# Kernel tuning notes

Hardware: AMD Instinct MI355X
Metric: run time of the kernel (lower is better)

Reference implementation:

```python
import jax, jax.numpy as jnp
import numpy as np

B, CIN, COUT, H, W = 2, 128, 128, 128, 256
KH, KW = 3, 3
CMID = 32  # COUT // low_factor


def setup_inputs() -> dict:
    key = jax.random.key(0)
    ks = jax.random.split(key, 7)
    x = jax.random.normal(ks[0], (B, CIN, H, W), jnp.float32)
    # torchvision deform_conv2d offset layout: [2*KH*KW, Ho, Wo], (dy, dx) per tap
    offset = jax.random.normal(ks[1], (2 * KH * KW, H, W), jnp.float32)
    weight = jax.random.normal(ks[2], (COUT, CIN, KH, KW), jnp.float32) * 0.05
    bias = jax.random.normal(ks[3], (COUT,), jnp.float32) * 0.01
    down_w = jax.random.normal(ks[4], (CMID, 2 * COUT), jnp.float32) * 0.05
    up_w = jax.random.normal(ks[5], (COUT, CMID), jnp.float32) * 0.05
    scale = jnp.float32(1.0)
    return dict(x=x, offset=offset, weight=weight, bias=bias,
                down_w=down_w, up_w=up_w, scale=scale)


def _deform_conv2d(x, offset, weight, bias):
    # stride=1, padding=1, dilation=1, groups=1 (matches init_conv config)
    Bn, C, Hh, Ww = x.shape
    Co, _, kh, kw = weight.shape
    K = kh * kw
    Ho, Wo = offset.shape[-2:]
    off = offset.reshape(K, 2, Ho, Wo)
    dy, dx = off[:, 0], off[:, 1]                      # [K, Ho, Wo]
    ki, kj = jnp.meshgrid(jnp.arange(kh), jnp.arange(kw), indexing='ij')
    ki = ki.reshape(K).astype(jnp.float32)
    kj = kj.reshape(K).astype(jnp.float32)
    i = jnp.arange(Ho, dtype=jnp.float32)
    j = jnp.arange(Wo, dtype=jnp.float32)
    PAD = 1.0
    py = i[None, :, None] - PAD + ki[:, None, None] + dy   # [K, Ho, Wo]
    px = j[None, None, :] - PAD + kj[:, None, None] + dx
    y0 = jnp.floor(py).astype(jnp.int32)
    x0 = jnp.floor(px).astype(jnp.int32)
    fy = py - y0.astype(py.dtype)
    fx = px - x0.astype(px.dtype)
    xf = x.reshape(Bn, C, Hh * Ww)

    def gather(yi, xi, w):
        # zero padding outside the image (torchvision semantics)
        valid = (yi >= 0) & (yi < Hh) & (xi >= 0) & (xi < Ww)
        yc = jnp.clip(yi, 0, Hh - 1)
        xc = jnp.clip(xi, 0, Ww - 1)
        idx = (yc * Ww + xc).reshape(-1)                   # [K*Ho*Wo]
        g = xf[:, :, idx].reshape(Bn, C, K, Ho, Wo)
        return g * (w * valid.astype(w.dtype))[None, None]

    val = gather(y0, x0, (1.0 - fy) * (1.0 - fx))
    val = val + gather(y0, x0 + 1, (1.0 - fy) * fx)
    val = val + gather(y0 + 1, x0, fy * (1.0 - fx))
    val = val + gather(y0 + 1, x0 + 1, fy * fx)
    out = jnp.einsum('bcnij,ocn->boij', val, weight.reshape(Co, C, K))
    return out + bias[None, :, None, None]


def reference(x, offset, weight, bias, down_w, up_w, scale):
    # h = original frozen conv (weights shared with the deform branch, ablation != wo_copy)
    h = jax.lax.conv_general_dilated(
        x, weight, window_strides=(1, 1), padding=[(1, 1), (1, 1)],
        dimension_numbers=('NCHW', 'OIHW', 'NCHW'))
    h = h + bias[None, :, None, None]
    dx = _deform_conv2d(x, offset, weight, bias)
    dx = jnp.concatenate([dx, h], axis=1)                  # mix == 'cat'
    lo = jnp.einsum('bcij,dc->bdij', dx, down_w)           # 1x1 conv_down
    up = jnp.einsum('bcij,dc->bdij', lo, up_w)             # 1x1 conv_up
    return h + scale * up
```

## Files before the change

kernel.cpp:

```cpp
#include <hip/hip_runtime.h>
#include <hip/hip_bf16.h>

typedef __attribute__((ext_vector_type(8))) short short8;
typedef __attribute__((ext_vector_type(8))) unsigned short ushort8;
typedef __attribute__((ext_vector_type(4))) float f32x4;
typedef __attribute__((ext_vector_type(4))) int int4v;
typedef __attribute__((ext_vector_type(4))) float float4v;
typedef __attribute__((ext_vector_type(2))) float float2v;
typedef __attribute__((ext_vector_type(4))) unsigned int uint4v;

#define HH 128
#define WW 256
#define CIN_ 128
#define COUT_ 128

__device__ __forceinline__ unsigned short f2bf(float f) {
  union { __hip_bfloat16 h; unsigned short u; } v;
  v.h = __float2bfloat16(f);
  return v.u;
}

__global__ __launch_bounds__(256) void k_pre1(
    const float* __restrict__ down_w, const float* __restrict__ weight,
    float* __restrict__ T,
    const float* __restrict__ x, unsigned short* __restrict__ xh,
    const float* __restrict__ offset, int4v* __restrict__ mo,
    float4v* __restrict__ mw) {
  __shared__ float tile[32 * 129];
  int bid = blockIdx.x;
  int tid = threadIdx.x;

  if (bid < 288) {
    int e = bid * 256 + tid;
    if (e >= 2 * 32 * 1152) return;
    int s = e / 36864, r = e % 36864, d = r / 1152, ck = r % 1152;
    float a = 0.f;
    #pragma unroll 4
    for (int p = 0; p < 128; ++p)
      a += down_w[d * 256 + s * 128 + p] * weight[p * 1152 + ck];
    T[e] = a;
  } else if (bid < 2336) {
    int idx = bid - 288;
    int b = idx >> 10, rem = idx & 1023;
    int y = rem >> 3, xg = (rem & 7) << 5;
    for (int it = tid; it < 32 * 128; it += 256) {
      int c = it >> 5, xi = it & 31;
      tile[xi * 129 + c] = x[(((size_t)b * 128 + c) * 128 + y) * 256 + xg + xi];
    }
    __syncthreads();
    for (int it = tid; it < 32 * 16; it += 256) {
      int xi = it >> 4, cs = it & 15;
      ushort8 v;
      #pragma unroll
      for (int e = 0; e < 8; ++e) v[e] = f2bf(tile[xi * 129 + cs * 8 + e]);
      *(ushort8*)(xh + (((size_t)b * 128 + y) * 256 + xg + xi) * 128 + cs * 8) = v;
    }
  } else {
    int e = (bid - 2336) * 256 + tid;
    if (e >= 9 * 128 * 256) return;
    int k = e >> 15, rem = e & 32767;
    int ii = rem >> 8, jj = rem & 255;
    float dy = offset[(2 * k) * 32768 + rem];
    float dx = offset[(2 * k + 1) * 32768 + rem];
    int ki = k / 3, kj = k % 3;
    float py = (float)(ii - 1 + ki) + dy;
    float px = (float)(jj - 1 + kj) + dx;
    float fy0 = floorf(py), fx0 = floorf(px);
    int y0 = (int)fy0, x0 = (int)fx0;
    float fy = py - fy0, fx = px - fx0;
    int ys[2] = {y0, y0 + 1};
    int xs_[2] = {x0, x0 + 1};
    float wy[2] = {1.f - fy, fy}, wx[2] = {1.f - fx, fx};
    int4v o;
    float4v w;
    #pragma unroll
    for (int cy = 0; cy < 2; ++cy) {
      #pragma unroll
      for (int cx = 0; cx < 2; ++cx) {
        int yy = ys[cy], xx = xs_[cx];
        bool valid = (yy >= 0) && (yy < HH) && (xx < WW) && (xx >= 0);
        int yc = min(max(yy, 0), HH - 1), xc = min(max(xx, 0), WW - 1);
        int off = (yc * WW + xc) * CIN_;
        float wv = valid ? wy[cy] * wx[cx] : 0.f;
        int ci = cy * 2 + cx;
        if (ci == 0) { o.x = off; w.x = wv; }
        else if (ci == 1) { o.y = off; w.y = wv; }
        else if (ci == 2) { o.z = off; w.z = wv; }
        else { o.w = off; w.w = wv; }
      }
    }
    mo[e] = o;
    mw[e] = w;
  }
}

__global__ __launch_bounds__(256) void k_pre2(
    const float* __restrict__ up_w, const float* __restrict__ weight,
    const float* __restrict__ T, const float* __restrict__ scale,
    unsigned short* __restrict__ wdef, unsigned short* __restrict__ wstd,
    const float* __restrict__ down_w, const float* __restrict__ bias,
    float* __restrict__ beff) {
  __shared__ float sd[32];
  int bid = blockIdx.x;
  int t = threadIdx.x;
  if (bid < 1152) {
    int e = bid * 256 + t;
    if (e >= 2 * 9 * 128 * 128) return;
    int s = e / 147456, r = e % 147456;
    int tap = r / 16384, o = (r / 128) % 128, c = r % 128;
    int ck = c * 9 + tap;
    const float* Ts = T + s * 36864;
    float a = 0.f;
    #pragma unroll
    for (int d = 0; d < 32; ++d) a += up_w[o * 32 + d] * Ts[d * 1152 + ck];
    float scl = scale[0];
    int idx = ((tap * 4 + (c >> 5)) * 128 + o) * 32 + (c & 31);
    if (s == 1) {
      wstd[idx] = f2bf(weight[o * 1152 + ck] + scl * a);
    } else {
      wdef[idx] = f2bf(scl * a);
    }
  } else {
    if (t < 32) {
      float a = 0.f;
      for (int p = 0; p < 128; ++p)
        a += (down_w[t * 256 + p] + down_w[t * 256 + 128 + p]) * bias[p];
      sd[t] = a;
    }
    __syncthreads();
    if (t < 128) {
      float a = 0.f;
      #pragma unroll
      for (int d = 0; d < 32; ++d) a += up_w[t * 32 + d] * sd[d];
      beff[t] = bias[t] + scale[0] * a;
    }
  }
}

__global__ __launch_bounds__(512, 4) void k_main(
    const unsigned short* __restrict__ xh,
    const int4v* __restrict__ mo, const float4v* __restrict__ mw,
    const unsigned short* __restrict__ wstd, const unsigned short* __restrict__ wdef,
    const float* __restrict__ beff, float* __restrict__ out) {
  __shared__ __align__(16) unsigned short sbuf[2][64 * 128];

  int orig = blockIdx.x;
  int t = ((orig & 7) << 7) + (orig >> 3);
  int b = t >> 9, i = (t >> 2) & 127, j0 = (t & 3) << 6;
  int tid = threadIdx.x;
  const unsigned short* xb = xh + (size_t)b * (HH * WW * CIN_);

  int wid = tid >> 6;
  bool producer = wid < 4;

  if (producer) {
    int ptid = tid;
    int slot = ptid & 15, pg = ptid >> 4;
    int ce = slot * 8;

    auto COMB = [&](uint4v* g, float4v w, int q, unsigned short* buf) {
      int p = q * 16 + pg;
      uint4v r;
      #pragma unroll
      for (int wi = 0; wi < 4; ++wi) {
        unsigned u0 = g[0][wi], u1 = g[1][wi], u2 = g[2][wi], u3 = g[3][wi];
        float2v f0 = {__builtin_bit_cast(float, u0 << 16), __builtin_bit_cast(float, u0 & 0xffff0000u)};
        float2v f1 = {__builtin_bit_cast(float, u1 << 16), __builtin_bit_cast(float, u1 & 0xffff0000u)};
        float2v f2 = {__builtin_bit_cast(float, u2 << 16), __builtin_bit_cast(float, u2 & 0xffff0000u)};
        float2v f3 = {__builtin_bit_cast(float, u3 << 16), __builtin_bit_cast(float, u3 & 0xffff0000u)};
        float2v s = w.x * f0 + w.y * f1 + w.z * f2 + w.w * f3;
        unsigned rr;
        asm("v_cvt_pk_bf16_f32 %0, %1, %2" : "=v"(rr) : "v"(s.x), "v"(s.y));
        r[wi] = rr;
      }
      *(uint4v*)((char*)buf + (p << 8) + ((slot ^ (p & 15)) << 4)) = r;
    };

    auto STAGE_DEF = [&](int tap, unsigned short* buf) {
      int4v o;
      float4v wq0, wq1;
      uint4v g0[4], g1[4];
      int mbase = (tap * HH + i) * WW + j0 + pg;

      o = mo[mbase]; wq0 = mw[mbase];
      g0[0] = *(const uint4v*)(xb + o.x + ce);
      g0[1] = *(const uint4v*)(xb + o.y + ce);
      g0[2] = *(const uint4v*)(xb + o.z + ce);
      g0[3] = *(const uint4v*)(xb + o.w + ce);
      o = mo[mbase + 16]; wq1 = mw[mbase + 16];
      g1[0] = *(const uint4v*)(xb + o.x + ce);
      g1[1] = *(const uint4v*)(xb + o.y + ce);
      g1[2] = *(const uint4v*)(xb + o.z + ce);
      g1[3] = *(const uint4v*)(xb + o.w + ce);

      COMB(g0, wq0, 0, buf);
      o = mo[mbase + 32]; wq0 = mw[mbase + 32];
      g0[0] = *(const uint4v*)(xb + o.x + ce);
      g0[1] = *(const uint4v*)(xb + o.y + ce);
      g0[2] = *(const uint4v*)(xb + o.z + ce);
      g0[3] = *(const uint4v*)(xb + o.w + ce);
      COMB(g1, wq1, 1, buf);
      o = mo[mbase + 48]; wq1 = mw[mbase + 48];
      g1[0] = *(const uint4v*)(xb + o.x + ce);
      g1[1] = *(const uint4v*)(xb + o.y + ce);
      g1[2] = *(const uint4v*)(xb + o.z + ce);
      g1[3] = *(const uint4v*)(xb + o.w + ce);
      COMB(g0, wq0, 2, buf);
      COMB(g1, wq1, 3, buf);
    };

    auto STAGE_STD = [&](int tap, unsigned short* buf) {
      int ki = tap / 3, kj = tap % 3;
      int gy = i - 1 + ki;
      bool oky = (unsigned)gy < (unsigned)HH;
      uint4v s[4];
      #pragma unroll
      for (int q = 0; q < 4; ++q) {
        int p = q * 16 + pg;
        int gx = j0 + p - 1 + kj;
        uint4v vv = {};
        if (oky && (unsigned)gx < (unsigned)WW)
          vv = *(const uint4v*)(xb + (size_t)(gy * WW + gx) * CIN_ + ce);
        s[q] = vv;
      }
      #pragma unroll
      for (int q = 0; q < 4; ++q) {
        int p = q * 16 + pg;
        *(uint4v*)((char*)buf + (p << 8) + ((slot ^ (p & 15)) << 4)) = s[q];
      }
    };

    STAGE_STD(0, sbuf[0]);
    __syncthreads();
    for (int v = 0; v < 18; ++v) {
      if (v < 17) {
        int nv = v + 1;
        if (nv & 1) STAGE_DEF(nv >> 1, sbuf[nv & 1]);
        else        STAGE_STD(nv >> 1, sbuf[nv & 1]);
      }
      __syncthreads();
    }
  } else {
    int lane = tid & 63;
    int cw = wid - 4;
    int obase = cw << 5;
    int lrow = lane & 15, lhi = lane >> 4;

    f32x4 acc[2][4] = {};

    __syncthreads();
    for (int v = 0; v < 18; ++v) {
      const unsigned short* cur = sbuf[v & 1];
      const unsigned short* wt = ((v & 1) ? wdef : wstd) + (size_t)(v >> 1) * 16384;
      short8 af[4][2];
      #pragma unroll
      for (int cc = 0; cc < 4; ++cc)
        #pragma unroll
        for (int am = 0; am < 2; ++am)
          af[cc][am] = *(const short8*)(wt + ((size_t)(cc * 128 + obase + am * 16 + lrow)) * 32 + lhi * 8);
      #pragma unroll
      for (int cc = 0; cc < 4; ++cc) {
        short8 bfr[4];
        #pragma unroll
        for (int bn = 0; bn < 4; ++bn) {
          int pp = bn * 16 + lrow;
          bfr[bn] = *(const short8*)((const char*)cur + (pp << 8) +
                                     (((cc * 4 + lhi) ^ lrow) << 4));
        }
        #pragma unroll
        for (int am = 0; am < 2; ++am)
          #pragma unroll
          for (int bn = 0; bn < 4; ++bn)
            acc[am][bn] = __builtin_amdgcn_mfma_f32_16x16x32_bf16(af[cc][am], bfr[bn], acc[am][bn], 0, 0, 0);
      }
      __syncthreads();
    }

    #pragma unroll
    for (int am = 0; am < 2; ++am) {
      #pragma unroll
      for (int bn = 0; bn < 4; ++bn) {
        int jg = j0 + bn * 16 + lrow;
        #pragma unroll
        for (int r = 0; r < 4; ++r) {
          int o = obase + am * 16 + lhi * 4 + r;
          out[(((size_t)b * COUT_ + o) * HH + i) * WW + jg] = acc[am][bn][r] + beff[o];
        }
      }
    }
  }
}

extern "C" void kernel_launch(void* const* d_in, const int* in_sizes, int n_in,
                              void* d_out, int out_size, void* d_ws, size_t ws_size,
                              hipStream_t stream) {
  const float* x      = (const float*)d_in[0];
  const float* offset = (const float*)d_in[1];
  const float* weight = (const float*)d_in[2];
  const float* bias   = (const float*)d_in[3];
  const float* down_w = (const float*)d_in[4];
  const float* up_w   = (const float*)d_in[5];
  const float* scale  = (const float*)d_in[6];
  float* out = (float*)d_out;

  char* ws = (char*)d_ws;
  unsigned short* xh   = (unsigned short*)(ws);
  int4v* mo            = (int4v*)(ws + 16777216);
  float4v* mw          = (float4v*)(ws + 21495808);
  unsigned short* wstd = (unsigned short*)(ws + 26214400);
  unsigned short* wdef = (unsigned short*)(ws + 26509312);
  float* T             = (float*)(ws + 26804224);
  float* beff          = (float*)(ws + 27099136);

  k_pre1<<<dim3(3488), dim3(256), 0, stream>>>(down_w, weight, T, x, xh, offset, mo, mw);
  k_pre2<<<dim3(1153), dim3(256), 0, stream>>>(up_w, weight, T, scale, wdef, wstd, down_w, bias, beff);
  k_main<<<dim3(1024), dim3(512), 0, stream>>>(xh, mo, mw, wstd, wdef, beff, out);
}
```

Baseline: 105.2 us.

## Process two output rows per block to reuse weight fragments

Each k_main block now computes two adjacent output rows instead of one, so the grid halves to 512 blocks. The producer stages both rows per tap into a doubled shared buffer, and the consumer reuses each weight A-fragment load across both row tiles. This cuts global weight-fragment traffic per output. In exchange it doubles shared memory (64KB per block), doubles accumulator registers, and halves block count, which may reduce occupancy and latency hiding on the gather-heavy producer path.

```diff
diff --git a/kernel.cpp b/kernel.cpp
--- a/kernel.cpp
+++ b/kernel.cpp
@@ -142,11 +142,12 @@
     const int4v* __restrict__ mo, const float4v* __restrict__ mw,
     const unsigned short* __restrict__ wstd, const unsigned short* __restrict__ wdef,
     const float* __restrict__ beff, float* __restrict__ out) {
-  __shared__ __align__(16) unsigned short sbuf[2][64 * 128];
+  __shared__ __align__(16) unsigned short sbuf[2][2][64 * 128];
 
   int orig = blockIdx.x;
-  int t = ((orig & 7) << 7) + (orig >> 3);
-  int b = t >> 9, i = (t >> 2) & 127, j0 = (t & 3) << 6;
+  int t = ((orig & 7) << 6) + (orig >> 3);
+  int b = t >> 8, ip = (t >> 2) & 63, j0 = (t & 3) << 6;
+  int i0 = ip << 1;
   int tid = threadIdx.x;
   const unsigned short* xb = xh + (size_t)b * (HH * WW * CIN_);
 
@@ -154,8 +155,7 @@
   bool producer = wid < 4;
 
   if (producer) {
-    int ptid = tid;
-    int slot = ptid & 15, pg = ptid >> 4;
+    int slot = tid & 15, pg = tid >> 4;
     int ce = slot * 8;
 
     auto COMB = [&](uint4v* g, float4v w, int q, unsigned short* buf) {
@@ -176,7 +176,7 @@
       *(uint4v*)((char*)buf + (p << 8) + ((slot ^ (p & 15)) << 4)) = r;
     };
 
-    auto STAGE_DEF = [&](int tap, unsigned short* buf) {
+    auto STAGE_DEF = [&](int tap, int i, unsigned short* buf) {
       int4v o;
       float4v wq0, wq1;
       uint4v g0[4], g1[4];
@@ -209,7 +209,7 @@
       COMB(g1, wq1, 3, buf);
     };
 
-    auto STAGE_STD = [&](int tap, unsigned short* buf) {
+    auto STAGE_STD = [&](int tap, int i, unsigned short* buf) {
       int ki = tap / 3, kj = tap % 3;
       int gy = i - 1 + ki;
       bool oky = (unsigned)gy < (unsigned)HH;
@@ -230,13 +230,19 @@
       }
     };
 
-    STAGE_STD(0, sbuf[0]);
+    STAGE_STD(0, i0, sbuf[0][0]);
+    STAGE_STD(0, i0 + 1, sbuf[0][1]);
     __syncthreads();
     for (int v = 0; v < 18; ++v) {
       if (v < 17) {
         int nv = v + 1;
-        if (nv & 1) STAGE_DEF(nv >> 1, sbuf[nv & 1]);
-        else        STAGE_STD(nv >> 1, sbuf[nv & 1]);
+        if (nv & 1) {
+          STAGE_DEF(nv >> 1, i0, sbuf[nv & 1][0]);
+          STAGE_DEF(nv >> 1, i0 + 1, sbuf[nv & 1][1]);
+        } else {
+          STAGE_STD(nv >> 1, i0, sbuf[nv & 1][0]);
+          STAGE_STD(nv >> 1, i0 + 1, sbuf[nv & 1][1]);
+        }
       }
       __syncthreads();
     }
@@ -246,11 +252,10 @@
     int obase = cw << 5;
     int lrow = lane & 15, lhi = lane >> 4;
 
-    f32x4 acc[2][4] = {};
+    f32x4 acc[2][2][4] = {};
 
     __syncthreads();
     for (int v = 0; v < 18; ++v) {
-      const unsigned short* cur = sbuf[v & 1];
       const unsigned short* wt = ((v & 1) ? wdef : wstd) + (size_t)(v >> 1) * 16384;
       short8 af[4][2];
       #pragma unroll
@@ -259,32 +264,40 @@
         for (int am = 0; am < 2; ++am)
           af[cc][am] = *(const short8*)(wt + ((size_t)(cc * 128 + obase + am * 16 + lrow)) * 32 + lhi * 8);
       #pragma unroll
-      for (int cc = 0; cc < 4; ++cc) {
-        short8 bfr[4];
+      for (int tile = 0; tile < 2; ++tile) {
+        const unsigned short* cur = sbuf[v & 1][tile];
+        #pragma unroll
+        for (int cc = 0; cc < 4; ++cc) {
+          short8 bfr[4];
+          #pragma unroll
+          for (int bn = 0; bn < 4; ++bn) {
+            int pp = bn * 16 + lrow;
+            bfr[bn] = *(const short8*)((const char*)cur + (pp << 8) +
+                                       (((cc * 4 + lhi) ^ lrow) << 4));
+          }
+          #pragma unroll
+          for (int am = 0; am < 2; ++am)
+            #pragma unroll
+            for (int bn = 0; bn < 4; ++bn)
+              acc[tile][am][bn] = __builtin_amdgcn_mfma_f32_16x16x32_bf16(af[cc][am], bfr[bn], acc[tile][am][bn], 0, 0, 0);
+        }
+      }
+      __syncthreads();
+    }
+
+    #pragma unroll
+    for (int tile = 0; tile < 2; ++tile) {
+      #pragma unroll
+      for (int am = 0; am < 2; ++am) {
         #pragma unroll
         for (int bn = 0; bn < 4; ++bn) {
-          int pp = bn * 16 + lrow;
-          bfr[bn] = *(const short8*)((const char*)cur + (pp << 8) +
-                                     (((cc * 4 + lhi) ^ lrow) << 4));
-        }
-        #pragma unroll
-        for (int am = 0; am < 2; ++am)
+          int jg = j0 + bn * 16 + lrow;
           #pragma unroll
-          for (int bn = 0; bn < 4; ++bn)
-            acc[am][bn] = __builtin_amdgcn_mfma_f32_16x16x32_bf16(af[cc][am], bfr[bn], acc[am][bn], 0, 0, 0);
-      }
-      __syncthreads();
-    }
-
-    #pragma unroll
-    for (int am = 0; am < 2; ++am) {
-      #pragma unroll
-      for (int bn = 0; bn < 4; ++bn) {
-        int jg = j0 + bn * 16 + lrow;
-        #pragma unroll
-        for (int r = 0; r < 4; ++r) {
-          int o = obase + am * 16 + lhi * 4 + r;
-          out[(((size_t)b * COUT_ + o) * HH + i) * WW + jg] = acc[am][bn][r] + beff[o];
+          for (int r = 0; r < 4; ++r) {
+            int o = obase + am * 16 + lhi * 4 + r;
+            out[(((size_t)b * COUT_ + o) * HH + (i0 + tile)) * WW + jg] =
+                acc[tile][am][bn][r] + beff[o];
+          }
         }
       }
     }
@@ -314,5 +327,5 @@
 
   k_pre1<<<dim3(3488), dim3(256), 0, stream>>>(down_w, weight, T, x, xh, offset, mo, mw);
   k_pre2<<<dim3(1153), dim3(256), 0, stream>>>(up_w, weight, T, scale, wdef, wstd, down_w, bias, beff);
-  k_main<<<dim3(1024), dim3(512), 0, stream>>>(xh, mo, mw, wstd, wdef, beff, out);
-}
+  k_main<<<dim3(512), dim3(512), 0, stream>>>(xh, mo, mw, wstd, wdef, beff, out);
+}
```

After: 93.88 us, median of 2. 1.12x faster.
